# Kernel tuning notes

Measured on AMD Instinct MI355X. Metric: run time of the kernel, lower is better.

## Reference

```python
import jax, jax.numpy as jnp
import numpy as np

EMBED = 256
HEADS = 8
HEAD_DIM = EMBED // HEADS
K = 7          # kernel_size
DIL = 1        # dilation
PAD = DIL * (K - 1) // 2  # 3
B, H, W = 4, 56, 56


def setup_inputs() -> dict:
    key = jax.random.key(0)
    ks = jax.random.split(key, 9)
    d = {"x": jax.random.normal(ks[0], (B, H, W, EMBED), jnp.float32)}
    for i, name in enumerate(["wq", "wk", "wv", "wo"]):
        d[name] = jax.random.normal(ks[1 + i], (EMBED, EMBED), jnp.float32) * 0.02
    for i, name in enumerate(["bq", "bk", "bv", "bo"]):
        d[name] = jax.random.normal(ks[5 + i], (EMBED,), jnp.float32) * 0.02
    return d


def _unfold(t):
    # t: [N, d, H, W] -> [N, d, K*K, H, W]; zero padding (matches F.unfold),
    # so out-of-bounds neighbors contribute logit 0, NOT -inf (faithful to source).
    h, w = t.shape[2], t.shape[3]
    tp = jnp.pad(t, ((0, 0), (0, 0), (PAD, PAD), (PAD, PAD)))
    patches = [tp[:, :, i * DIL:i * DIL + h, j * DIL:j * DIL + w]
               for i in range(K) for j in range(K)]  # fixed K*K=49 offsets
    return jnp.stack(patches, axis=2)


def reference(x, wq, bq, wk, bk, wv, bv, wo, bo):
    b, h, w, c = x.shape
    scale = HEAD_DIM ** -0.5
    q = x @ wq.T + bq
    k = x @ wk.T + bk
    v = x @ wv.T + bv

    def to_nh(t):  # [B,H,W,C] -> [B*heads, head_dim, H, W]
        return t.reshape(b, h, w, HEADS, HEAD_DIM).transpose(0, 3, 4, 1, 2).reshape(b * HEADS, HEAD_DIM, h, w)

    q, k, v = to_nh(q), to_nh(k), to_nh(v)
    k_unf = _unfold(k)  # [N, d, K2, H, W]
    v_unf = _unfold(v)
    logits = jnp.einsum('ndhw,ndkhw->nkhw', q, k_unf) * scale  # [N, K2, H, W]
    attn = jax.nn.softmax(logits, axis=1)
    out = jnp.einsum('nkhw,ndkhw->ndhw', attn, v_unf)  # [N, d, H, W]
    out = out.reshape(b, HEADS, HEAD_DIM, h, w).transpose(0, 3, 4, 1, 2).reshape(b, h, w, c)
    return out @ wo.T + bo
```

## Files before the change

kernel.cpp:

```cpp
#include <hip/hip_runtime.h>

typedef unsigned int u32;
typedef unsigned short u16;
typedef _Float16 f16;
typedef __attribute__((ext_vector_type(8))) _Float16 f16x8;
typedef __attribute__((ext_vector_type(4))) float f32x4;

#define T_TOK 12544
#define EMB   256
#define IMG   56
#define SCALE2 0.25503486f
#define HALO  196
#define KSTR  40
#define VTSTR 208
#define PSTR  136

__device__ __forceinline__ u16 f16b(float f) {
    const f16 h = (f16)f;
    return __builtin_bit_cast(u16, h);
}

#define GLD16(g, l) __builtin_amdgcn_global_load_lds( \
    (const __attribute__((address_space(1))) u32*)(g), \
    (__attribute__((address_space(3))) u32*)(l), 16, 0, 0)

__global__ __launch_bounds__(256) void convert_kernel(
    const float* __restrict__ x, const float* __restrict__ wq, const float* __restrict__ wk,
    const float* __restrict__ wv, const float* __restrict__ wo,
    u16* __restrict__ xb, u16* __restrict__ wsh, u16* __restrict__ woh) {
    const int i = blockIdx.x * 256 + threadIdx.x;
    const int NX4 = T_TOK * EMB / 4;
    if (i < NX4) {
        const float4 f = ((const float4*)x)[i];
        ushort4 hv;
        hv.x = f16b(f.x); hv.y = f16b(f.y); hv.z = f16b(f.z); hv.w = f16b(f.w);
        ((ushort4*)xb)[i] = hv;
    } else {
        const int j = i - NX4;
        const int w = j >> 14, widx = j & 16383;
        const float* src = (w == 0) ? wq : (w == 1) ? wk : (w == 2) ? wv : wo;
        const float4 f = ((const float4*)src)[widx];
        ushort4 hv;
        hv.x = f16b(f.x); hv.y = f16b(f.y); hv.z = f16b(f.z); hv.w = f16b(f.w);
        if (w < 3) ((ushort4*)wsh)[(w << 14) + widx] = hv;
        else       ((ushort4*)woh)[widx] = hv;
    }
}

__global__ __launch_bounds__(256) void qkv_mfma(
    const u16* __restrict__ xb, const u16* __restrict__ wsh,
    const float* __restrict__ bq, const float* __restrict__ bk, const float* __restrict__ bv,
    u16* __restrict__ qb, u16* __restrict__ kb, u16* __restrict__ vb) {
    __shared__ __attribute__((aligned(16))) u16 sA[2][128 * 32];
    __shared__ __attribute__((aligned(16))) u16 sB[2][128 * 32];
    const int bid = blockIdx.y * 6 + blockIdx.x;
    const int xcd = bid & 7, loc = bid >> 3;
    const int work = (xcd < 4 ? xcd * 74 : 296 + (xcd - 4) * 73) + loc;
    const int nBase = (work % 6) * 128;
    const int mBase = (work / 6) * 128;
    const int tid = threadIdx.x, wv = tid >> 6, ln = tid & 63;
    const int lrow = ln & 15, lqd = ln >> 4;
    const int wr = wv >> 1, wc = wv & 1;
    const int rA = tid >> 2, kcA = tid & 3;
    const size_t gA = (size_t)(mBase + rA) * EMB + kcA * 8;
    const size_t gB = (size_t)(nBase + rA) * EMB + kcA * 8;
    const int lA = wv * 512;

    f32x4 acc[4][4];
    #pragma unroll
    for (int mi = 0; mi < 4; ++mi)
        #pragma unroll
        for (int ni = 0; ni < 4; ++ni) acc[mi][ni] = (f32x4){0.f, 0.f, 0.f, 0.f};

    GLD16(xb  + gA,            &sA[0][lA]);
    GLD16(xb  + gA + 64 * EMB, &sA[0][2048 + lA]);
    GLD16(wsh + gB,            &sB[0][lA]);
    GLD16(wsh + gB + 64 * EMB, &sB[0][2048 + lA]);

    for (int kt = 0; kt < 8; ++kt) {
        const int b = kt & 1;
        __syncthreads();
        if (kt < 7) {
            const int k0 = (kt + 1) * 32;
            GLD16(xb  + gA + k0,            &sA[b ^ 1][lA]);
            GLD16(xb  + gA + k0 + 64 * EMB, &sA[b ^ 1][2048 + lA]);
            GLD16(wsh + gB + k0,            &sB[b ^ 1][lA]);
            GLD16(wsh + gB + k0 + 64 * EMB, &sB[b ^ 1][2048 + lA]);
        }
        f16x8 af[4], bfr[4];
        #pragma unroll
        for (int mi = 0; mi < 4; ++mi)
            af[mi] = *(const f16x8*)&sA[b][(wr * 64 + mi * 16 + lrow) * 32 + lqd * 8];
        #pragma unroll
        for (int ni = 0; ni < 4; ++ni)
            bfr[ni] = *(const f16x8*)&sB[b][(wc * 64 + ni * 16 + lrow) * 32 + lqd * 8];
        #pragma unroll
        for (int mi = 0; mi < 4; ++mi)
            #pragma unroll
            for (int ni = 0; ni < 4; ++ni)
                acc[mi][ni] = __builtin_amdgcn_mfma_f32_16x16x32_f16(af[mi], bfr[ni], acc[mi][ni], 0, 0, 0);
    }

    const int which = nBase >> 8;
    const float* bias = (which == 0) ? bq : (which == 1) ? bk : bv;
    u16* dst = (which == 0) ? qb : (which == 1) ? kb : vb;
    #pragma unroll
    for (int ni = 0; ni < 4; ++ni) {
        const int cg = (nBase & 255) + wc * 64 + ni * 16;
        const int head = cg >> 5;
        const int d = (cg & 31) + lrow;
        const float bz = bias[cg + lrow];
        u16* dh = dst + (size_t)head * T_TOK * 32;
        #pragma unroll
        for (int mi = 0; mi < 4; ++mi) {
            #pragma unroll
            for (int r = 0; r < 4; ++r) {
                const int row = mBase + wr * 64 + mi * 16 + lqd * 4 + r;
                dh[(size_t)row * 32 + d] = f16b(acc[mi][ni][r] + bz);
            }
        }
    }
}

__global__ __launch_bounds__(256) void out_mfma(
    const u16* __restrict__ ao, const u16* __restrict__ woh,
    const float* __restrict__ bo, float* __restrict__ out) {
    __shared__ __attribute__((aligned(16))) u16 sA[2][64 * 32];
    __shared__ __attribute__((aligned(16))) u16 sB[2][64 * 32];
    const int bid = blockIdx.y * 4 + blockIdx.x;
    const int work = (bid & 7) * 98 + (bid >> 3);
    const int nBase = (work & 3) * 64;
    const int mBase = (work >> 2) * 64;
    const int tid = threadIdx.x, wv = tid >> 6, ln = tid & 63;
    const int lrow = ln & 15, lqd = ln >> 4;
    const int rA = tid >> 2, kcA = tid & 3;
    const size_t gA = (size_t)(mBase + rA) * EMB + kcA * 8;
    const size_t gB = (size_t)(nBase + rA) * EMB + kcA * 8;
    const int lA = wv * 512;

    f32x4 acc[4];
    #pragma unroll
    for (int mi = 0; mi < 4; ++mi) acc[mi] = (f32x4){0.f, 0.f, 0.f, 0.f};

    GLD16(ao  + gA, &sA[0][lA]);
    GLD16(woh + gB, &sB[0][lA]);

    for (int kt = 0; kt < 8; ++kt) {
        const int b = kt & 1;
        __syncthreads();
        if (kt < 7) {
            const int k0 = (kt + 1) * 32;
            GLD16(ao  + gA + k0, &sA[b ^ 1][lA]);
            GLD16(woh + gB + k0, &sB[b ^ 1][lA]);
        }
        f16x8 af[4];
        #pragma unroll
        for (int mi = 0; mi < 4; ++mi)
            af[mi] = *(const f16x8*)&sA[b][(mi * 16 + lrow) * 32 + lqd * 8];
        const f16x8 bf = *(const f16x8*)&sB[b][(wv * 16 + lrow) * 32 + lqd * 8];
        #pragma unroll
        for (int mi = 0; mi < 4; ++mi)
            acc[mi] = __builtin_amdgcn_mfma_f32_16x16x32_f16(af[mi], bf, acc[mi], 0, 0, 0);
    }

    const int ncol = nBase + wv * 16 + lrow;
    const float bz = bo[ncol];
    #pragma unroll
    for (int mi = 0; mi < 4; ++mi) {
        #pragma unroll
        for (int r = 0; r < 4; ++r) {
            const int row = mBase + mi * 16 + lqd * 4 + r;
            out[(size_t)row * EMB + ncol] = acc[mi][r] + bz;
        }
    }
}

__global__ __launch_bounds__(256, 5) void attn_kernel(
    const u16* __restrict__ qb, const u16* __restrict__ kb, const u16* __restrict__ vb,
    u16* __restrict__ ao) {
    __shared__ __attribute__((aligned(16))) u16 smem[15360];
    u16* sVT = smem;
    u16* sK  = smem + 6656;
    u16* sP  = smem + 6656;

    const int tid = threadIdx.x;
    const int w = tid >> 6, ln = tid & 63;
    const int lrow = ln & 15, lqd = ln >> 4;
    const int img = blockIdx.z >> 3, head = blockIdx.z & 7;
    const int ty0 = blockIdx.y * 8, tx0 = blockIdx.x * 8;
    const int base8 = (28 * w) & ~7;

    const u16* kbh = kb + (size_t)head * (T_TOK * 32);
    const u16* vbh = vb + (size_t)head * (T_TOK * 32);
    const u16* qbh = qb + (size_t)head * (T_TOK * 32);

    for (int i = tid; i < 1664; i += 256) {
        const int mv = (i >= 832) ? 1 : 0;
        const int ii = i - 832 * mv;
        const int p = ii >> 2, c = ii & 3;
        const int pyh = p / 14, pxh = p - pyh * 14;
        const int gy = ty0 - 3 + pyh, gx = tx0 - 3 + pxh;
        const bool ok = (p < HALO) & ((unsigned)gy < 56u) & ((unsigned)gx < 56u);
        const size_t tt = (size_t)((img * IMG + gy) * IMG + gx) * 32;
        if (!mv) {
            u16* dstk = sK + p * KSTR + c * 8;
            if (ok) {
                *(uint4*)dstk = *(const uint4*)(kbh + tt + c * 8);
            } else {
                *(uint4*)dstk = (uint4){0u, 0u, 0u, 0u};
            }
        } else {
            u16* dv = sVT + (c * 8) * VTSTR + p;
            if (ok) {
                const uint4 u = *(const uint4*)(vbh + tt + c * 8);
                dv[0 * VTSTR] = (u16)(u.x & 0xffffu);
                dv[1 * VTSTR] = (u16)(u.x >> 16);
                dv[2 * VTSTR] = (u16)(u.y & 0xffffu);
                dv[3 * VTSTR] = (u16)(u.y >> 16);
                dv[4 * VTSTR] = (u16)(u.z & 0xffffu);
                dv[5 * VTSTR] = (u16)(u.z >> 16);
                dv[6 * VTSTR] = (u16)(u.w & 0xffffu);
                dv[7 * VTSTR] = (u16)(u.w >> 16);
            } else {
                #pragma unroll
                for (int j = 0; j < 8; ++j) dv[j * VTSTR] = 0;
            }
        }
    }

    const int qpy = 2 * w + (lrow >> 3), qpx = lrow & 7;
    const size_t qtok = ((size_t)img * IMG + ty0 + qpy) * IMG + tx0 + qpx;
    const f16x8 aq = *(const f16x8*)&qbh[qtok * 32 + lqd * 8];
    __syncthreads();

    f32x4 ct[8];
    #pragma unroll
    for (int t = 0; t < 8; ++t) ct[t] = (f32x4){0.f, 0.f, 0.f, 0.f};
    #pragma unroll
    for (int t = 0; t < 8; ++t) {
        const f16x8 bk = *(const f16x8*)&sK[(base8 + t * 16 + lrow) * KSTR + lqd * 8];
        ct[t] = __builtin_amdgcn_mfma_f32_16x16x32_f16(bk, aq, ct[t], 0, 0, 0);
    }

    float ssum = 0.f;
    #pragma unroll
    for (int t = 0; t < 8; ++t) {
        #pragma unroll
        for (int r = 0; r < 4; ++r) {
            const int col = base8 + t * 16 + lqd * 4 + r;
            const int hy = col / 14, hx = col - 14 * hy;
            const bool ok = ((unsigned)(hy - qpy) < 7u) &
                            ((unsigned)(hx - qpx) < 7u) & (col < HALO);
            const float e = ok ? exp2f(ct[t][r] * SCALE2) : 0.f;
            ct[t][r] = e;
            ssum += e;
        }
    }
    ssum += __shfl_xor(ssum, 16);
    ssum += __shfl_xor(ssum, 32);
    const float inv = 1.0f / ssum;

    __syncthreads();

    u16* sPw = sP + w * 16 * PSTR;
    #pragma unroll
    for (int t = 0; t < 8; ++t) {
        ushort4 pw;
        pw.x = f16b(ct[t][0]);
        pw.y = f16b(ct[t][1]);
        pw.z = f16b(ct[t][2]);
        pw.w = f16b(ct[t][3]);
        *(ushort4*)&sPw[lrow * PSTR + t * 16 + lqd * 4] = pw;
    }

    f32x4 o0 = (f32x4){0.f, 0.f, 0.f, 0.f};
    f32x4 o1 = (f32x4){0.f, 0.f, 0.f, 0.f};
    #pragma unroll
    for (int ks = 0; ks < 4; ++ks) {
        const f16x8 ap  = *(const f16x8*)&sPw[lrow * PSTR + ks * 32 + lqd * 8];
        const f16x8 av0 = *(const f16x8*)&sVT[lrow * VTSTR + base8 + ks * 32 + lqd * 8];
        const f16x8 av1 = *(const f16x8*)&sVT[(16 + lrow) * VTSTR + base8 + ks * 32 + lqd * 8];
        o0 = __builtin_amdgcn_mfma_f32_16x16x32_f16(av0, ap, o0, 0, 0, 0);
        o1 = __builtin_amdgcn_mfma_f32_16x16x32_f16(av1, ap, o1, 0, 0, 0);
    }

    const size_t base = qtok * EMB + head * 32;
    ushort4 s0, s1;
    s0.x = f16b(o0[0] * inv); s0.y = f16b(o0[1] * inv);
    s0.z = f16b(o0[2] * inv); s0.w = f16b(o0[3] * inv);
    s1.x = f16b(o1[0] * inv); s1.y = f16b(o1[1] * inv);
    s1.z = f16b(o1[2] * inv); s1.w = f16b(o1[3] * inv);
    *(ushort4*)&ao[base + lqd * 4]      = s0;
    *(ushort4*)&ao[base + 16 + lqd * 4] = s1;
}

extern "C" void kernel_launch(void* const* d_in, const int* in_sizes, int n_in,
                              void* d_out, int out_size, void* d_ws, size_t ws_size,
                              hipStream_t stream) {
    const float* x  = (const float*)d_in[0];
    const float* wq = (const float*)d_in[1];
    const float* wk = (const float*)d_in[2];
    const float* wv = (const float*)d_in[3];
    const float* wo = (const float*)d_in[4];
    const float* bq = (const float*)d_in[5];
    const float* bk = (const float*)d_in[6];
    const float* bv = (const float*)d_in[7];
    const float* bo = (const float*)d_in[8];
    float* out = (float*)d_out;

    char* ws = (char*)d_ws;
    u16* xb  = (u16*)(ws);
    u16* qb  = (u16*)(ws +  6422528);
    u16* kb  = (u16*)(ws + 12845056);
    u16* vb  = (u16*)(ws + 19267584);
    u16* ao  = (u16*)(ws + 25690112);
    u16* wsh = (u16*)(ws + 32112640);
    u16* woh = (u16*)(ws + 32505856);

    convert_kernel<<<3392, 256, 0, stream>>>(x, wq, wk, wv, wo, xb, wsh, woh);
    qkv_mfma<<<dim3(6, 98), 256, 0, stream>>>(xb, wsh, bq, bk, bv, qb, kb, vb);
    attn_kernel<<<dim3(7, 7, 32), 256, 0, stream>>>(qb, kb, vb, ao);
    out_mfma<<<dim3(4, 196), 256, 0, stream>>>(ao, woh, bo, out);
}
```

Before: 120.8 us.

## Fuse fp32-to-fp16 conversion into GEMM loaders and pair V transpose stores

Removes the separate conversion kernel. The QKV and output GEMMs now load fp32 x and weights directly, converting to fp16 in registers before writing to LDS, with the global loads issued before the MFMA step and the LDS stores after it. This drops one launch and one full write and read of a half-precision copy of x. The cost is that the GEMMs read twice the bytes for x and the weights and lose the async global-to-LDS path. The attention kernel's V halo transpose also handles two tokens per thread and writes packed 32-bit LDS words instead of 16-bit scatter stores.

```diff
diff --git a/kernel.cpp b/kernel.cpp
--- a/kernel.cpp
+++ b/kernel.cpp
@@ -19,36 +19,23 @@
     const f16 h = (f16)f;
     return __builtin_bit_cast(u16, h);
 }
+__device__ __forceinline__ u32 pk2(float lo, float hi) {
+    return (u32)f16b(lo) | ((u32)f16b(hi) << 16);
+}
+__device__ __forceinline__ uint4 pk16(const float4 a, const float4 b) {
+    uint4 r;
+    r.x = pk2(a.x, a.y); r.y = pk2(a.z, a.w);
+    r.z = pk2(b.x, b.y); r.w = pk2(b.z, b.w);
+    return r;
+}
 
 #define GLD16(g, l) __builtin_amdgcn_global_load_lds( \
     (const __attribute__((address_space(1))) u32*)(g), \
     (__attribute__((address_space(3))) u32*)(l), 16, 0, 0)
 
-__global__ __launch_bounds__(256) void convert_kernel(
-    const float* __restrict__ x, const float* __restrict__ wq, const float* __restrict__ wk,
-    const float* __restrict__ wv, const float* __restrict__ wo,
-    u16* __restrict__ xb, u16* __restrict__ wsh, u16* __restrict__ woh) {
-    const int i = blockIdx.x * 256 + threadIdx.x;
-    const int NX4 = T_TOK * EMB / 4;
-    if (i < NX4) {
-        const float4 f = ((const float4*)x)[i];
-        ushort4 hv;
-        hv.x = f16b(f.x); hv.y = f16b(f.y); hv.z = f16b(f.z); hv.w = f16b(f.w);
-        ((ushort4*)xb)[i] = hv;
-    } else {
-        const int j = i - NX4;
-        const int w = j >> 14, widx = j & 16383;
-        const float* src = (w == 0) ? wq : (w == 1) ? wk : (w == 2) ? wv : wo;
-        const float4 f = ((const float4*)src)[widx];
-        ushort4 hv;
-        hv.x = f16b(f.x); hv.y = f16b(f.y); hv.z = f16b(f.z); hv.w = f16b(f.w);
-        if (w < 3) ((ushort4*)wsh)[(w << 14) + widx] = hv;
-        else       ((ushort4*)woh)[widx] = hv;
-    }
-}
-
 __global__ __launch_bounds__(256) void qkv_mfma(
-    const u16* __restrict__ xb, const u16* __restrict__ wsh,
+    const float* __restrict__ xf,
+    const float* __restrict__ wq, const float* __restrict__ wk, const float* __restrict__ wv,
     const float* __restrict__ bq, const float* __restrict__ bk, const float* __restrict__ bv,
     u16* __restrict__ qb, u16* __restrict__ kb, u16* __restrict__ vb) {
     __shared__ __attribute__((aligned(16))) u16 sA[2][128 * 32];
@@ -58,13 +45,18 @@
     const int work = (xcd < 4 ? xcd * 74 : 296 + (xcd - 4) * 73) + loc;
     const int nBase = (work % 6) * 128;
     const int mBase = (work / 6) * 128;
-    const int tid = threadIdx.x, wv = tid >> 6, ln = tid & 63;
+    const int tid = threadIdx.x, wv_ = tid >> 6, ln = tid & 63;
     const int lrow = ln & 15, lqd = ln >> 4;
-    const int wr = wv >> 1, wc = wv & 1;
-    const int rA = tid >> 2, kcA = tid & 3;
-    const size_t gA = (size_t)(mBase + rA) * EMB + kcA * 8;
-    const size_t gB = (size_t)(nBase + rA) * EMB + kcA * 8;
-    const int lA = wv * 512;
+    const int wr = wv_ >> 1, wc = wv_ & 1;
+
+    const int which = nBase >> 8;
+    const float* wsrc = (which == 0) ? wq : (which == 1) ? wk : wv;
+    const int nrow0 = nBase & 255;
+
+    const int arow = tid >> 2, acol = (tid & 3) * 8;
+    const float* gAf = xf   + (size_t)(mBase + arow) * EMB + acol;
+    const float* gBf = wsrc + (size_t)(nrow0 + arow) * EMB + acol;
+    const int so = tid * 8;
 
     f32x4 acc[4][4];
     #pragma unroll
@@ -72,20 +64,35 @@
         #pragma unroll
         for (int ni = 0; ni < 4; ++ni) acc[mi][ni] = (f32x4){0.f, 0.f, 0.f, 0.f};
 
-    GLD16(xb  + gA,            &sA[0][lA]);
-    GLD16(xb  + gA + 64 * EMB, &sA[0][2048 + lA]);
-    GLD16(wsh + gB,            &sB[0][lA]);
-    GLD16(wsh + gB + 64 * EMB, &sB[0][2048 + lA]);
+    {
+        const float4 ra0 = *(const float4*)(gAf);
+        const float4 ra1 = *(const float4*)(gAf + 4);
+        const float4 ra2 = *(const float4*)(gAf + 64 * EMB);
+        const float4 ra3 = *(const float4*)(gAf + 64 * EMB + 4);
+        const float4 rb0 = *(const float4*)(gBf);
+        const float4 rb1 = *(const float4*)(gBf + 4);
+        const float4 rb2 = *(const float4*)(gBf + 64 * EMB);
+        const float4 rb3 = *(const float4*)(gBf + 64 * EMB + 4);
+        *(uint4*)&sA[0][so]        = pk16(ra0, ra1);
+        *(uint4*)&sA[0][2048 + so] = pk16(ra2, ra3);
+        *(uint4*)&sB[0][so]        = pk16(rb0, rb1);
+        *(uint4*)&sB[0][2048 + so] = pk16(rb2, rb3);
+    }
 
     for (int kt = 0; kt < 8; ++kt) {
         const int b = kt & 1;
         __syncthreads();
+        float4 ra0, ra1, ra2, ra3, rb0, rb1, rb2, rb3;
         if (kt < 7) {
             const int k0 = (kt + 1) * 32;
-            GLD16(xb  + gA + k0,            &sA[b ^ 1][lA]);
-            GLD16(xb  + gA + k0 + 64 * EMB, &sA[b ^ 1][2048 + lA]);
-            GLD16(wsh + gB + k0,            &sB[b ^ 1][lA]);
-            GLD16(wsh + gB + k0 + 64 * EMB, &sB[b ^ 1][2048 + lA]);
+            ra0 = *(const float4*)(gAf + k0);
+            ra1 = *(const float4*)(gAf + k0 + 4);
+            ra2 = *(const float4*)(gAf + k0 + 64 * EMB);
+            ra3 = *(const float4*)(gAf + k0 + 64 * EMB + 4);
+            rb0 = *(const float4*)(gBf + k0);
+            rb1 = *(const float4*)(gBf + k0 + 4);
+            rb2 = *(const float4*)(gBf + k0 + 64 * EMB);
+            rb3 = *(const float4*)(gBf + k0 + 64 * EMB + 4);
         }
         f16x8 af[4], bfr[4];
         #pragma unroll
@@ -99,14 +106,19 @@
             #pragma unroll
             for (int ni = 0; ni < 4; ++ni)
                 acc[mi][ni] = __builtin_amdgcn_mfma_f32_16x16x32_f16(af[mi], bfr[ni], acc[mi][ni], 0, 0, 0);
-    }
-
-    const int which = nBase >> 8;
+        if (kt < 7) {
+            *(uint4*)&sA[b ^ 1][so]        = pk16(ra0, ra1);
+            *(uint4*)&sA[b ^ 1][2048 + so] = pk16(ra2, ra3);
+            *(uint4*)&sB[b ^ 1][so]        = pk16(rb0, rb1);
+            *(uint4*)&sB[b ^ 1][2048 + so] = pk16(rb2, rb3);
+        }
+    }
+
     const float* bias = (which == 0) ? bq : (which == 1) ? bk : bv;
     u16* dst = (which == 0) ? qb : (which == 1) ? kb : vb;
     #pragma unroll
     for (int ni = 0; ni < 4; ++ni) {
-        const int cg = (nBase & 255) + wc * 64 + ni * 16;
+        const int cg = nrow0 + wc * 64 + ni * 16;
         const int head = cg >> 5;
         const int d = (cg & 31) + lrow;
         const float bz = bias[cg + lrow];
@@ -123,7 +135,7 @@
 }
 
 __global__ __launch_bounds__(256) void out_mfma(
-    const u16* __restrict__ ao, const u16* __restrict__ woh,
+    const u16* __restrict__ ao, const float* __restrict__ wo,
     const float* __restrict__ bo, float* __restrict__ out) {
     __shared__ __attribute__((aligned(16))) u16 sA[2][64 * 32];
     __shared__ __attribute__((aligned(16))) u16 sB[2][64 * 32];
@@ -131,39 +143,51 @@
     const int work = (bid & 7) * 98 + (bid >> 3);
     const int nBase = (work & 3) * 64;
     const int mBase = (work >> 2) * 64;
-    const int tid = threadIdx.x, wv = tid >> 6, ln = tid & 63;
+    const int tid = threadIdx.x, wv_ = tid >> 6, ln = tid & 63;
     const int lrow = ln & 15, lqd = ln >> 4;
     const int rA = tid >> 2, kcA = tid & 3;
     const size_t gA = (size_t)(mBase + rA) * EMB + kcA * 8;
-    const size_t gB = (size_t)(nBase + rA) * EMB + kcA * 8;
-    const int lA = wv * 512;
+    const int lA = wv_ * 512;
+
+    const int brow = tid >> 2, bcol = (tid & 3) * 8;
+    const float* gBf = wo + (size_t)(nBase + brow) * EMB + bcol;
+    const int so = tid * 8;
 
     f32x4 acc[4];
     #pragma unroll
     for (int mi = 0; mi < 4; ++mi) acc[mi] = (f32x4){0.f, 0.f, 0.f, 0.f};
 
-    GLD16(ao  + gA, &sA[0][lA]);
-    GLD16(woh + gB, &sB[0][lA]);
+    GLD16(ao + gA, &sA[0][lA]);
+    {
+        const float4 rb0 = *(const float4*)(gBf);
+        const float4 rb1 = *(const float4*)(gBf + 4);
+        *(uint4*)&sB[0][so] = pk16(rb0, rb1);
+    }
 
     for (int kt = 0; kt < 8; ++kt) {
         const int b = kt & 1;
         __syncthreads();
+        float4 rb0, rb1;
         if (kt < 7) {
             const int k0 = (kt + 1) * 32;
-            GLD16(ao  + gA + k0, &sA[b ^ 1][lA]);
-            GLD16(woh + gB + k0, &sB[b ^ 1][lA]);
+            GLD16(ao + gA + k0, &sA[b ^ 1][lA]);
+            rb0 = *(const float4*)(gBf + k0);
+            rb1 = *(const float4*)(gBf + k0 + 4);
         }
         f16x8 af[4];
         #pragma unroll
         for (int mi = 0; mi < 4; ++mi)
             af[mi] = *(const f16x8*)&sA[b][(mi * 16 + lrow) * 32 + lqd * 8];
-        const f16x8 bf = *(const f16x8*)&sB[b][(wv * 16 + lrow) * 32 + lqd * 8];
+        const f16x8 bf = *(const f16x8*)&sB[b][(wv_ * 16 + lrow) * 32 + lqd * 8];
         #pragma unroll
         for (int mi = 0; mi < 4; ++mi)
             acc[mi] = __builtin_amdgcn_mfma_f32_16x16x32_f16(af[mi], bf, acc[mi], 0, 0, 0);
-    }
-
-    const int ncol = nBase + wv * 16 + lrow;
+        if (kt < 7) {
+            *(uint4*)&sB[b ^ 1][so] = pk16(rb0, rb1);
+        }
+    }
+
+    const int ncol = nBase + wv_ * 16 + lrow;
     const float bz = bo[ncol];
     #pragma unroll
     for (int mi = 0; mi < 4; ++mi) {
@@ -194,37 +218,42 @@
     const u16* vbh = vb + (size_t)head * (T_TOK * 32);
     const u16* qbh = qb + (size_t)head * (T_TOK * 32);
 
-    for (int i = tid; i < 1664; i += 256) {
-        const int mv = (i >= 832) ? 1 : 0;
-        const int ii = i - 832 * mv;
-        const int p = ii >> 2, c = ii & 3;
-        const int pyh = p / 14, pxh = p - pyh * 14;
-        const int gy = ty0 - 3 + pyh, gx = tx0 - 3 + pxh;
-        const bool ok = (p < HALO) & ((unsigned)gy < 56u) & ((unsigned)gx < 56u);
-        const size_t tt = (size_t)((img * IMG + gy) * IMG + gx) * 32;
-        if (!mv) {
+    for (int i = tid; i < 1248; i += 256) {
+        if (i < 832) {
+            const int p = i >> 2, c = i & 3;
+            const int pyh = p / 14, pxh = p - pyh * 14;
+            const int gy = ty0 - 3 + pyh, gx = tx0 - 3 + pxh;
+            const bool ok = (p < HALO) & ((unsigned)gy < 56u) & ((unsigned)gx < 56u);
             u16* dstk = sK + p * KSTR + c * 8;
             if (ok) {
+                const size_t tt = (size_t)((img * IMG + gy) * IMG + gx) * 32;
                 *(uint4*)dstk = *(const uint4*)(kbh + tt + c * 8);
             } else {
                 *(uint4*)dstk = (uint4){0u, 0u, 0u, 0u};
             }
         } else {
-            u16* dv = sVT + (c * 8) * VTSTR + p;
-            if (ok) {
-                const uint4 u = *(const uint4*)(vbh + tt + c * 8);
-                dv[0 * VTSTR] = (u16)(u.x & 0xffffu);
-                dv[1 * VTSTR] = (u16)(u.x >> 16);
-                dv[2 * VTSTR] = (u16)(u.y & 0xffffu);
-                dv[3 * VTSTR] = (u16)(u.y >> 16);
-                dv[4 * VTSTR] = (u16)(u.z & 0xffffu);
-                dv[5 * VTSTR] = (u16)(u.z >> 16);
-                dv[6 * VTSTR] = (u16)(u.w & 0xffffu);
-                dv[7 * VTSTR] = (u16)(u.w >> 16);
-            } else {
-                #pragma unroll
-                for (int j = 0; j < 8; ++j) dv[j * VTSTR] = 0;
-            }
+            const int j = i - 832;
+            const int pp = j >> 2, c = j & 3;
+            const int p0 = pp * 2;
+            const int pyh = p0 / 14, pxh = p0 - pyh * 14;
+            const int gy = ty0 - 3 + pyh, gx = tx0 - 3 + pxh;
+            const bool oky = (p0 < HALO) & ((unsigned)gy < 56u);
+            const bool ok0 = oky & ((unsigned)gx < 56u);
+            const bool ok1 = oky & ((unsigned)(gx + 1) < 56u);
+            const long long tt = (long long)((img * IMG + gy) * IMG + gx) * 32;
+            const uint4 u0 = ok0 ? *(const uint4*)(vbh + tt + c * 8)
+                                 : (uint4){0u, 0u, 0u, 0u};
+            const uint4 u1 = ok1 ? *(const uint4*)(vbh + tt + 32 + c * 8)
+                                 : (uint4){0u, 0u, 0u, 0u};
+            u16* dv = sVT + (c * 8) * VTSTR + p0;
+            *(u32*)&dv[0 * VTSTR] = (u0.x & 0xffffu) | (u1.x << 16);
+            *(u32*)&dv[1 * VTSTR] = (u0.x >> 16)     | (u1.x & 0xffff0000u);
+            *(u32*)&dv[2 * VTSTR] = (u0.y & 0xffffu) | (u1.y << 16);
+            *(u32*)&dv[3 * VTSTR] = (u0.y >> 16)     | (u1.y & 0xffff0000u);
+            *(u32*)&dv[4 * VTSTR] = (u0.z & 0xffffu) | (u1.z << 16);
+            *(u32*)&dv[5 * VTSTR] = (u0.z >> 16)     | (u1.z & 0xffff0000u);
+            *(u32*)&dv[6 * VTSTR] = (u0.w & 0xffffu) | (u1.w << 16);
+            *(u32*)&dv[7 * VTSTR] = (u0.w >> 16)     | (u1.w & 0xffff0000u);
         }
     }
 
@@ -309,16 +338,12 @@
     float* out = (float*)d_out;
 
     char* ws = (char*)d_ws;
-    u16* xb  = (u16*)(ws);
-    u16* qb  = (u16*)(ws +  6422528);
-    u16* kb  = (u16*)(ws + 12845056);
-    u16* vb  = (u16*)(ws + 19267584);
-    u16* ao  = (u16*)(ws + 25690112);
-    u16* wsh = (u16*)(ws + 32112640);
-    u16* woh = (u16*)(ws + 32505856);
-
-    convert_kernel<<<3392, 256, 0, stream>>>(x, wq, wk, wv, wo, xb, wsh, woh);
-    qkv_mfma<<<dim3(6, 98), 256, 0, stream>>>(xb, wsh, bq, bk, bv, qb, kb, vb);
+    u16* qb = (u16*)(ws);
+    u16* kb = (u16*)(ws +  6422528);
+    u16* vb = (u16*)(ws + 12845056);
+    u16* ao = (u16*)(ws + 19267584);
+
+    qkv_mfma<<<dim3(6, 98), 256, 0, stream>>>(x, wq, wk, wv, bq, bk, bv, qb, kb, vb);
     attn_kernel<<<dim3(7, 7, 32), 256, 0, stream>>>(qb, kb, vb, ao);
-    out_mfma<<<dim3(4, 196), 256, 0, stream>>>(ao, woh, bo, out);
-}
+    out_mfma<<<dim3(4, 196), 256, 0, stream>>>(ao, wo, bo, out);
+}
```

Measured after the change: 116.1 us. 1.04x faster.
